# Performance work log

Hardware: AMD Instinct MI355X
Metric: run time of the kernel (lower is better)

## Reference

```python
import jax, jax.numpy as jnp
import numpy as np

MAX_THRESHOLD = 0.95


def leaky_clamp(x, lo, hi, slope):
    # identity inside [lo, hi], linear with `slope` outside
    return jnp.where(x < lo, lo + slope * (x - lo),
                     jnp.where(x > hi, hi + slope * (x - hi), x))


def or_gate_layer(x, W, tau_adder):
    # x: (B, in), W: (out, in)
    in_f = W.shape[1]
    tau_floor = float(np.log(in_f - 1) + np.log(MAX_THRESHOLD) - np.log(1.0 - MAX_THRESHOLD))
    tau = tau_floor + jax.nn.leaky_relu(tau_adder, negative_slope=0.05)
    aw = leaky_clamp(W, 0.0, 1.0, 0.1)           # (out, in)
    z = x[:, None, :] * aw[None, :, :]           # (B, out, in) broadcast
    p = jax.nn.softmax(tau * z, axis=-1)         # tau-scaled softmax over in
    return jnp.sum(p * z, axis=-1)               # (B, out)


def setup_inputs() -> dict:
    key = jax.random.key(0)
    ks = jax.random.split(key, 9)
    input_dim = 512
    layer_dims = [1024, 512, 256, 128]
    x = jax.random.uniform(ks[0], (128, input_dim), dtype=jnp.float32)
    in_dim = input_dim * 2
    out = {"x": x}
    for i, out_dim in enumerate(layer_dims):
        out[f"W{i}"] = jax.random.normal(ks[1 + i], (out_dim, in_dim), dtype=jnp.float32)
        out[f"tau{i}"] = jnp.zeros((), dtype=jnp.float32)
        in_dim = out_dim  # only_inverter=True
    return out


def reference(x, W0, W1, W2, W3, tau0, tau1, tau2, tau3):
    h = jnp.concatenate([x, 1.0 - x], axis=-1)   # pass_invert
    for W, t in ((W0, tau0), (W1, tau1), (W2, tau2), (W3, tau3)):
        h = 1.0 - or_gate_layer(h, W, t)         # only_inverter: invert after every layer
    return h
```

## Files before the change

### kernel.cpp

```cpp
#include <hip/hip_runtime.h>
#include <math.h>

#if defined(__has_builtin)
#  if __has_builtin(__builtin_amdgcn_exp2f)
#    define EXP2F(x) __builtin_amdgcn_exp2f(x)
#  endif
#endif
#ifndef EXP2F
#  define EXP2F(x) __expf(0.69314718055994530942f * (x))
#endif

template <int IN, int OUT, int BB, bool FIRST>
__launch_bounds__(256)
__global__ void or_layer(const float* __restrict__ hin,
                         const float* __restrict__ W,
                         const float* __restrict__ tau_ptr,
                         float* __restrict__ hout,
                         float tau_floor) {
  constexpr int OBB = 2;
  constexpr int NIT = IN / 64;
  constexpr int nOT = OUT / 32;

  const int lane = threadIdx.x & 63;
  const int wid  = threadIdx.x >> 6;
  const int il   = lane & 15;
  const int og   = lane >> 4;

  const int ot = blockIdx.x % nOT;
  const int bt = blockIdx.x / nOT;
  const int b0 = bt * BB;
  const int o0 = ot * 32 + wid * 8 + og * OBB;

  const float ta  = tau_ptr[0];
  const float tau = tau_floor + (ta >= 0.0f ? ta : 0.05f * ta);
  const float c2  = tau * 1.44269504088896340736f;

  const float4* __restrict__ Wv = (const float4*)W;
  const float4* __restrict__ Hv = (const float4*)hin;

  float s[BB][OBB], t[BB][OBB];
#pragma unroll
  for (int r = 0; r < BB; ++r)
#pragma unroll
    for (int c = 0; c < OBB; ++c) { s[r][c] = 0.0f; t[r][c] = 0.0f; }

#pragma unroll 2
  for (int ic = 0; ic < NIT; ++ic) {
    const int i4 = ic * 16 + il;

    float hc[BB][4];
    if (FIRST) {
      constexpr int HALF4 = IN / 8;
      if (i4 < HALF4) {
#pragma unroll
        for (int r = 0; r < BB; ++r) {
          float4 v = Hv[(b0 + r) * HALF4 + i4];
          hc[r][0] = v.x; hc[r][1] = v.y; hc[r][2] = v.z; hc[r][3] = v.w;
        }
      } else {
#pragma unroll
        for (int r = 0; r < BB; ++r) {
          float4 v = Hv[(b0 + r) * HALF4 + (i4 - HALF4)];
          hc[r][0] = 1.0f - v.x; hc[r][1] = 1.0f - v.y;
          hc[r][2] = 1.0f - v.z; hc[r][3] = 1.0f - v.w;
        }
      }
    } else {
#pragma unroll
      for (int r = 0; r < BB; ++r) {
        float4 v = Hv[(b0 + r) * (IN / 4) + i4];
        hc[r][0] = v.x; hc[r][1] = v.y; hc[r][2] = v.z; hc[r][3] = v.w;
      }
    }

    float cw[OBB][4];
#pragma unroll
    for (int c = 0; c < OBB; ++c) {
      float4 v = Wv[(o0 + c) * (IN / 4) + i4];
      float wj[4] = {v.x, v.y, v.z, v.w};
#pragma unroll
      for (int j = 0; j < 4; ++j) {
        const float m  = fminf(fmaxf(wj[j], 0.0f), 1.0f);
        const float aw = fmaf(0.1f, wj[j] - m, m);
        cw[c][j] = c2 * aw;
      }
    }

#pragma unroll
    for (int r = 0; r < BB; ++r)
#pragma unroll
      for (int c = 0; c < OBB; ++c)
#pragma unroll
        for (int j = 0; j < 4; ++j) {
          const float arg = cw[c][j] * hc[r][j];
          const float e   = EXP2F(arg);
          s[r][c] += e;
          t[r][c]  = fmaf(arg, e, t[r][c]);
        }
  }

#pragma unroll
  for (int m = 1; m < 16; m <<= 1) {
#pragma unroll
    for (int r = 0; r < BB; ++r)
#pragma unroll
      for (int c = 0; c < OBB; ++c) {
        s[r][c] += __shfl_xor(s[r][c], m, 64);
        t[r][c] += __shfl_xor(t[r][c], m, 64);
      }
  }

  if (il == 0) {
    const float inv_c2 = 1.0f / c2;
#pragma unroll
    for (int r = 0; r < BB; ++r)
#pragma unroll
      for (int c = 0; c < OBB; ++c) {
        const float out = t[r][c] / s[r][c] * inv_c2;
        hout[(b0 + r) * OUT + (o0 + c)] = 1.0f - out;
      }
  }
}

extern "C" void kernel_launch(void* const* d_in, const int* in_sizes, int n_in,
                              void* d_out, int out_size, void* d_ws, size_t ws_size,
                              hipStream_t stream) {
  const float* x    = (const float*)d_in[0];
  const float* W0   = (const float*)d_in[1];
  const float* tau0 = (const float*)d_in[2];
  const float* W1   = (const float*)d_in[3];
  const float* tau1 = (const float*)d_in[4];
  const float* W2   = (const float*)d_in[5];
  const float* tau2 = (const float*)d_in[6];
  const float* W3   = (const float*)d_in[7];
  const float* tau3 = (const float*)d_in[8];

  float* h1  = (float*)d_ws;
  float* h2  = h1 + 128 * 1024;
  float* h3  = h2 + 128 * 512;
  float* out = (float*)d_out;

  const double LOGR = 2.9444389791664403;
  const float tf1024 = (float)(log(1023.0) + LOGR);
  const float tf512  = (float)(log(511.0)  + LOGR);
  const float tf256  = (float)(log(255.0)  + LOGR);

  or_layer<1024, 1024, 8, true ><<<32 * 16, 256, 0, stream>>>(x,  W0, tau0, h1,  tf1024);
  or_layer<1024,  512, 8, false><<<16 * 16, 256, 0, stream>>>(h1, W1, tau1, h2,  tf1024);
  or_layer< 512,  256, 4, false><<< 8 * 32, 256, 0, stream>>>(h2, W2, tau2, h3,  tf512);
  or_layer< 256,  128, 2, false><<< 4 * 64, 256, 0, stream>>>(h3, W3, tau3, out, tf256);
}
```

Measured before the change: 124.7 us.

## Split exp2 between hardware transcendental unit and packed-FP32 polynomial emulation

Rewrites the inner loop on float2 vectors so the weight clamp, the multiplies and the accumulations can map to packed FP32 instructions. Half of the exponentials still use the hardware exp2 instruction. The other half use a degree-3 polynomial with exponent bit manipulation built from packed FMAs, which balances work between the transcendental unit and the vector ALU. It also drops the loop unroll to 1, and the launch grid sizes are only written as literals. The polynomial exp2 is less accurate than the hardware one and has no overflow or underflow guard.

```diff
diff --git a/kernel.cpp b/kernel.cpp
--- a/kernel.cpp
+++ b/kernel.cpp
@@ -9,6 +9,49 @@
 #ifndef EXP2F
 #  define EXP2F(x) __expf(0.69314718055994530942f * (x))
 #endif
+
+typedef float v2f __attribute__((ext_vector_type(2)));
+typedef int   v2i __attribute__((ext_vector_type(2)));
+
+__device__ __forceinline__ v2f v2fma(v2f a, v2f b, v2f c) {
+#if defined(__has_builtin) && __has_builtin(__builtin_elementwise_fma)
+  return __builtin_elementwise_fma(a, b, c);
+#else
+  v2f r; r.x = fmaf(a.x, b.x, c.x); r.y = fmaf(a.y, b.y, c.y); return r;
+#endif
+}
+__device__ __forceinline__ v2f v2max(v2f a, v2f b) {
+#if defined(__has_builtin) && __has_builtin(__builtin_elementwise_max)
+  return __builtin_elementwise_max(a, b);
+#else
+  v2f r; r.x = fmaxf(a.x, b.x); r.y = fmaxf(a.y, b.y); return r;
+#endif
+}
+__device__ __forceinline__ v2f v2min(v2f a, v2f b) {
+#if defined(__has_builtin) && __has_builtin(__builtin_elementwise_min)
+  return __builtin_elementwise_min(a, b);
+#else
+  v2f r; r.x = fminf(a.x, b.x); r.y = fminf(a.y, b.y); return r;
+#endif
+}
+
+__device__ __forceinline__ v2f fast_exp2_v2(v2f x) {
+  const v2f M  = {12582912.0f, 12582912.0f};
+  const v2f C2 = {0.055504109f, 0.055504109f};
+  const v2f C1 = {0.24022651f, 0.24022651f};
+  const v2f C0 = {0.69314718f, 0.69314718f};
+  const v2f ONE = {1.0f, 1.0f};
+  v2f y = x + M;
+  v2f n = y - M;
+  v2f f = x - n;
+  v2f p = v2fma(f, C2, C1);
+  p = v2fma(f, p, C0);
+  p = v2fma(f, p, ONE);
+  v2i yi = __builtin_bit_cast(v2i, y);
+  v2i pi = __builtin_bit_cast(v2i, p);
+  v2i r  = (yi << 23) + pi;
+  return __builtin_bit_cast(v2f, r);
+}
 
 template <int IN, int OUT, int BB, bool FIRST>
 __launch_bounds__(256)
@@ -34,79 +77,109 @@
   const float ta  = tau_ptr[0];
   const float tau = tau_floor + (ta >= 0.0f ? ta : 0.05f * ta);
   const float c2  = tau * 1.44269504088896340736f;
+  const v2f   c2v = {c2, c2};
+  const v2f   ZERO = {0.0f, 0.0f};
+  const v2f   ONE  = {1.0f, 1.0f};
+  const v2f   SLOPE = {0.1f, 0.1f};
 
   const float4* __restrict__ Wv = (const float4*)W;
   const float4* __restrict__ Hv = (const float4*)hin;
 
-  float s[BB][OBB], t[BB][OBB];
+  v2f s[BB][OBB], t[BB][OBB];
 #pragma unroll
   for (int r = 0; r < BB; ++r)
 #pragma unroll
-    for (int c = 0; c < OBB; ++c) { s[r][c] = 0.0f; t[r][c] = 0.0f; }
-
-#pragma unroll 2
+    for (int c = 0; c < OBB; ++c) {
+      s[r][c] = ZERO;
+      t[r][c] = ZERO;
+    }
+
+#pragma unroll 1
   for (int ic = 0; ic < NIT; ++ic) {
     const int i4 = ic * 16 + il;
 
-    float hc[BB][4];
+    v2f hp[BB][2];
     if (FIRST) {
       constexpr int HALF4 = IN / 8;
       if (i4 < HALF4) {
 #pragma unroll
         for (int r = 0; r < BB; ++r) {
           float4 v = Hv[(b0 + r) * HALF4 + i4];
-          hc[r][0] = v.x; hc[r][1] = v.y; hc[r][2] = v.z; hc[r][3] = v.w;
+          v2f a; a.x = v.x; a.y = v.y;
+          v2f b; b.x = v.z; b.y = v.w;
+          hp[r][0] = a; hp[r][1] = b;
         }
       } else {
 #pragma unroll
         for (int r = 0; r < BB; ++r) {
           float4 v = Hv[(b0 + r) * HALF4 + (i4 - HALF4)];
-          hc[r][0] = 1.0f - v.x; hc[r][1] = 1.0f - v.y;
-          hc[r][2] = 1.0f - v.z; hc[r][3] = 1.0f - v.w;
+          v2f a; a.x = v.x; a.y = v.y;
+          v2f b; b.x = v.z; b.y = v.w;
+          hp[r][0] = ONE - a; hp[r][1] = ONE - b;
         }
       }
     } else {
 #pragma unroll
       for (int r = 0; r < BB; ++r) {
         float4 v = Hv[(b0 + r) * (IN / 4) + i4];
-        hc[r][0] = v.x; hc[r][1] = v.y; hc[r][2] = v.z; hc[r][3] = v.w;
-      }
-    }
-
-    float cw[OBB][4];
+        v2f a; a.x = v.x; a.y = v.y;
+        v2f b; b.x = v.z; b.y = v.w;
+        hp[r][0] = a; hp[r][1] = b;
+      }
+    }
+
+    v2f cw[OBB][2];
 #pragma unroll
     for (int c = 0; c < OBB; ++c) {
       float4 v = Wv[(o0 + c) * (IN / 4) + i4];
-      float wj[4] = {v.x, v.y, v.z, v.w};
-#pragma unroll
-      for (int j = 0; j < 4; ++j) {
-        const float m  = fminf(fmaxf(wj[j], 0.0f), 1.0f);
-        const float aw = fmaf(0.1f, wj[j] - m, m);
-        cw[c][j] = c2 * aw;
+      v2f wp0; wp0.x = v.x; wp0.y = v.y;
+      v2f wp1; wp1.x = v.z; wp1.y = v.w;
+      v2f wp[2] = {wp0, wp1};
+#pragma unroll
+      for (int q = 0; q < 2; ++q) {
+        v2f m  = v2min(v2max(wp[q], ZERO), ONE);
+        v2f aw = v2fma(wp[q] - m, SLOPE, m);
+        cw[c][q] = aw * c2v;
       }
     }
 
 #pragma unroll
     for (int r = 0; r < BB; ++r)
 #pragma unroll
-      for (int c = 0; c < OBB; ++c)
-#pragma unroll
-        for (int j = 0; j < 4; ++j) {
-          const float arg = cw[c][j] * hc[r][j];
-          const float e   = EXP2F(arg);
+      for (int c = 0; c < OBB; ++c) {
+        {
+          v2f arg = cw[c][0] * hp[r][0];
+          v2f e;
+          e.x = EXP2F(arg.x);
+          e.y = EXP2F(arg.y);
           s[r][c] += e;
-          t[r][c]  = fmaf(arg, e, t[r][c]);
-        }
+          t[r][c]  = v2fma(arg, e, t[r][c]);
+        }
+        {
+          v2f arg = cw[c][1] * hp[r][1];
+          v2f e   = fast_exp2_v2(arg);
+          s[r][c] += e;
+          t[r][c]  = v2fma(arg, e, t[r][c]);
+        }
+      }
   }
 
+  float ss[BB][OBB], tt[BB][OBB];
+#pragma unroll
+  for (int r = 0; r < BB; ++r)
+#pragma unroll
+    for (int c = 0; c < OBB; ++c) {
+      ss[r][c] = s[r][c].x + s[r][c].y;
+      tt[r][c] = t[r][c].x + t[r][c].y;
+    }
 #pragma unroll
   for (int m = 1; m < 16; m <<= 1) {
 #pragma unroll
     for (int r = 0; r < BB; ++r)
 #pragma unroll
       for (int c = 0; c < OBB; ++c) {
-        s[r][c] += __shfl_xor(s[r][c], m, 64);
-        t[r][c] += __shfl_xor(t[r][c], m, 64);
+        ss[r][c] += __shfl_xor(ss[r][c], m, 64);
+        tt[r][c] += __shfl_xor(tt[r][c], m, 64);
       }
   }
 
@@ -116,7 +189,7 @@
     for (int r = 0; r < BB; ++r)
 #pragma unroll
       for (int c = 0; c < OBB; ++c) {
-        const float out = t[r][c] / s[r][c] * inv_c2;
+        const float out = tt[r][c] / ss[r][c] * inv_c2;
         hout[(b0 + r) * OUT + (o0 + c)] = 1.0f - out;
       }
   }
@@ -145,8 +218,8 @@
   const float tf512  = (float)(log(511.0)  + LOGR);
   const float tf256  = (float)(log(255.0)  + LOGR);
 
-  or_layer<1024, 1024, 8, true ><<<32 * 16, 256, 0, stream>>>(x,  W0, tau0, h1,  tf1024);
-  or_layer<1024,  512, 8, false><<<16 * 16, 256, 0, stream>>>(h1, W1, tau1, h2,  tf1024);
-  or_layer< 512,  256, 4, false><<< 8 * 32, 256, 0, stream>>>(h2, W2, tau2, h3,  tf512);
-  or_layer< 256,  128, 2, false><<< 4 * 64, 256, 0, stream>>>(h3, W3, tau3, out, tf256);
-}
+  or_layer<1024, 1024, 8, true ><<<512, 256, 0, stream>>>(x,  W0, tau0, h1,  tf1024);
+  or_layer<1024,  512, 8, false><<<256, 256, 0, stream>>>(h1, W1, tau1, h2,  tf1024);
+  or_layer< 512,  256, 4, false><<<256, 256, 0, stream>>>(h2, W2, tau2, h3,  tf512);
+  or_layer< 256,  128, 2, false><<<256, 256, 0, stream>>>(h3, W3, tau3, out, tf256);
+}
```

Result: slower. 137.8 us (+10.6%).

## Fuse all layers into one cooperative kernel with precomputed scaled weights

Applied to the files above, without the earlier changes.

Replaces the four per-layer launches with a single cooperative kernel that uses grid-wide syncs between layers. A prologue pass writes the clamped, tau-scaled weights to a workspace buffer, so the inner loops no longer redo the leaky clamp per batch tile. The cost is an extra full read and write of all weights, plus four grid barriers. If the cooperative launch fails, it falls back to a prep kernel followed by separate layer kernels.

```diff
diff --git a/kernel.cpp b/kernel.cpp
--- a/kernel.cpp
+++ b/kernel.cpp
@@ -1,5 +1,8 @@
 #include <hip/hip_runtime.h>
+#include <hip/hip_cooperative_groups.h>
 #include <math.h>
+
+namespace cg = cooperative_groups;
 
 #if defined(__has_builtin)
 #  if __has_builtin(__builtin_amdgcn_exp2f)
@@ -10,32 +13,53 @@
 #  define EXP2F(x) __expf(0.69314718055994530942f * (x))
 #endif
 
+
+__device__ __forceinline__ float calc_c2(const float* tau_ptr, float tf) {
+  const float ta  = tau_ptr[0];
+  const float tau = tf + (ta >= 0.0f ? ta : 0.05f * ta);
+  return tau * 1.44269504088896340736f;
+}
+
+__device__ __forceinline__ void prep_cw(const float* __restrict__ W,
+                                        float* __restrict__ cw,
+                                        int n4, float c2, int gtid, int gsz) {
+  const float4* __restrict__ Wv = (const float4*)W;
+  float4* __restrict__ Cv = (float4*)cw;
+  for (int k = gtid; k < n4; k += gsz) {
+    float4 v = Wv[k];
+    float w[4] = {v.x, v.y, v.z, v.w};
+    float o[4];
+#pragma unroll
+    for (int j = 0; j < 4; ++j) {
+      const float m  = fminf(fmaxf(w[j], 0.0f), 1.0f);
+      const float aw = fmaf(0.1f, w[j] - m, m);
+      o[j] = c2 * aw;
+    }
+    float4 r; r.x = o[0]; r.y = o[1]; r.z = o[2]; r.w = o[3];
+    Cv[k] = r;
+  }
+}
+
 template <int IN, int OUT, int BB, bool FIRST>
-__launch_bounds__(256)
-__global__ void or_layer(const float* __restrict__ hin,
-                         const float* __restrict__ W,
-                         const float* __restrict__ tau_ptr,
-                         float* __restrict__ hout,
-                         float tau_floor) {
+__device__ __forceinline__ void layer_body(const float* __restrict__ hin,
+                                           const float* __restrict__ cw,
+                                           float* __restrict__ hout,
+                                           float c2, int bid, int tid) {
   constexpr int OBB = 2;
   constexpr int NIT = IN / 64;
   constexpr int nOT = OUT / 32;
 
-  const int lane = threadIdx.x & 63;
-  const int wid  = threadIdx.x >> 6;
+  const int lane = tid & 63;
+  const int wid  = tid >> 6;
   const int il   = lane & 15;
   const int og   = lane >> 4;
 
-  const int ot = blockIdx.x % nOT;
-  const int bt = blockIdx.x / nOT;
+  const int ot = bid % nOT;
+  const int bt = bid / nOT;
   const int b0 = bt * BB;
   const int o0 = ot * 32 + wid * 8 + og * OBB;
 
-  const float ta  = tau_ptr[0];
-  const float tau = tau_floor + (ta >= 0.0f ? ta : 0.05f * ta);
-  const float c2  = tau * 1.44269504088896340736f;
-
-  const float4* __restrict__ Wv = (const float4*)W;
+  const float4* __restrict__ Cv = (const float4*)cw;
   const float4* __restrict__ Hv = (const float4*)hin;
 
   float s[BB][OBB], t[BB][OBB];
@@ -73,17 +97,11 @@
       }
     }
 
-    float cw[OBB][4];
+    float a[OBB][4];
 #pragma unroll
     for (int c = 0; c < OBB; ++c) {
-      float4 v = Wv[(o0 + c) * (IN / 4) + i4];
-      float wj[4] = {v.x, v.y, v.z, v.w};
-#pragma unroll
-      for (int j = 0; j < 4; ++j) {
-        const float m  = fminf(fmaxf(wj[j], 0.0f), 1.0f);
-        const float aw = fmaf(0.1f, wj[j] - m, m);
-        cw[c][j] = c2 * aw;
-      }
+      float4 v = Cv[(o0 + c) * (IN / 4) + i4];
+      a[c][0] = v.x; a[c][1] = v.y; a[c][2] = v.z; a[c][3] = v.w;
     }
 
 #pragma unroll
@@ -92,7 +110,7 @@
       for (int c = 0; c < OBB; ++c)
 #pragma unroll
         for (int j = 0; j < 4; ++j) {
-          const float arg = cw[c][j] * hc[r][j];
+          const float arg = a[c][j] * hc[r][j];
           const float e   = EXP2F(arg);
           s[r][c] += e;
           t[r][c]  = fmaf(arg, e, t[r][c]);
@@ -120,6 +138,69 @@
         hout[(b0 + r) * OUT + (o0 + c)] = 1.0f - out;
       }
   }
+}
+
+__launch_bounds__(256, 2)
+__global__ void or_fused(const float* __restrict__ x,
+                         const float* __restrict__ W0, const float* __restrict__ W1,
+                         const float* __restrict__ W2, const float* __restrict__ W3,
+                         const float* __restrict__ tau0, const float* __restrict__ tau1,
+                         const float* __restrict__ tau2, const float* __restrict__ tau3,
+                         float* __restrict__ h1, float* __restrict__ h2,
+                         float* __restrict__ h3, float* __restrict__ out,
+                         float* __restrict__ cw0, float* __restrict__ cw1,
+                         float* __restrict__ cw2, float* __restrict__ cw3,
+                         float tf0, float tf1, float tf2, float tf3) {
+  cg::grid_group grid = cg::this_grid();
+  const int tid  = threadIdx.x;
+  const int bid  = blockIdx.x;
+  const int gtid = bid * 256 + tid;
+  const int gsz  = gridDim.x * 256;
+
+  const float c2_0 = calc_c2(tau0, tf0);
+  const float c2_1 = calc_c2(tau1, tf1);
+  const float c2_2 = calc_c2(tau2, tf2);
+  const float c2_3 = calc_c2(tau3, tf3);
+
+  prep_cw(W0, cw0, 1024 * 1024 / 4, c2_0, gtid, gsz);
+  prep_cw(W1, cw1,  512 * 1024 / 4, c2_1, gtid, gsz);
+  prep_cw(W2, cw2,  256 *  512 / 4, c2_2, gtid, gsz);
+  prep_cw(W3, cw3,  128 *  256 / 4, c2_3, gtid, gsz);
+  grid.sync();
+
+  layer_body<1024, 1024, 8, true >(x, cw0, h1, c2_0, bid, tid);
+  grid.sync();
+  if (bid < 256) layer_body<1024, 512, 8, false>(h1, cw1, h2, c2_1, bid, tid);
+  grid.sync();
+  if (bid < 256) layer_body<512, 256, 4, false>(h2, cw2, h3, c2_2, bid, tid);
+  grid.sync();
+  if (bid < 256) layer_body<256, 128, 2, false>(h3, cw3, out, c2_3, bid, tid);
+}
+
+__launch_bounds__(256)
+__global__ void prep_all(const float* __restrict__ W0, const float* __restrict__ W1,
+                         const float* __restrict__ W2, const float* __restrict__ W3,
+                         const float* __restrict__ tau0, const float* __restrict__ tau1,
+                         const float* __restrict__ tau2, const float* __restrict__ tau3,
+                         float* __restrict__ cw0, float* __restrict__ cw1,
+                         float* __restrict__ cw2, float* __restrict__ cw3,
+                         float tf0, float tf1, float tf2, float tf3) {
+  const int gtid = blockIdx.x * 256 + threadIdx.x;
+  const int gsz  = gridDim.x * 256;
+  prep_cw(W0, cw0, 1024 * 1024 / 4, calc_c2(tau0, tf0), gtid, gsz);
+  prep_cw(W1, cw1,  512 * 1024 / 4, calc_c2(tau1, tf1), gtid, gsz);
+  prep_cw(W2, cw2,  256 *  512 / 4, calc_c2(tau2, tf2), gtid, gsz);
+  prep_cw(W3, cw3,  128 *  256 / 4, calc_c2(tau3, tf3), gtid, gsz);
+}
+
+template <int IN, int OUT, int BB, bool FIRST>
+__launch_bounds__(256)
+__global__ void or_layer_k(const float* __restrict__ hin,
+                           const float* __restrict__ cw,
+                           const float* __restrict__ tau_ptr,
+                           float* __restrict__ hout, float tf) {
+  layer_body<IN, OUT, BB, FIRST>(hin, cw, hout, calc_c2(tau_ptr, tf),
+                                 blockIdx.x, threadIdx.x);
 }
 
 extern "C" void kernel_launch(void* const* d_in, const int* in_sizes, int n_in,
@@ -138,15 +219,34 @@
   float* h1  = (float*)d_ws;
   float* h2  = h1 + 128 * 1024;
   float* h3  = h2 + 128 * 512;
+  float* cw0 = h3 + 128 * 256;
+  float* cw1 = cw0 + 1024 * 1024;
+  float* cw2 = cw1 + 512 * 1024;
+  float* cw3 = cw2 + 256 * 512;
   float* out = (float*)d_out;
 
   const double LOGR = 2.9444389791664403;
-  const float tf1024 = (float)(log(1023.0) + LOGR);
-  const float tf512  = (float)(log(511.0)  + LOGR);
-  const float tf256  = (float)(log(255.0)  + LOGR);
-
-  or_layer<1024, 1024, 8, true ><<<32 * 16, 256, 0, stream>>>(x,  W0, tau0, h1,  tf1024);
-  or_layer<1024,  512, 8, false><<<16 * 16, 256, 0, stream>>>(h1, W1, tau1, h2,  tf1024);
-  or_layer< 512,  256, 4, false><<< 8 * 32, 256, 0, stream>>>(h2, W2, tau2, h3,  tf512);
-  or_layer< 256,  128, 2, false><<< 4 * 64, 256, 0, stream>>>(h3, W3, tau3, out, tf256);
-}
+  float tf0 = (float)(log(1023.0) + LOGR);
+  float tf1 = (float)(log(1023.0) + LOGR);
+  float tf2 = (float)(log(511.0)  + LOGR);
+  float tf3 = (float)(log(255.0)  + LOGR);
+
+  void* args[] = {
+    (void*)&x,
+    (void*)&W0, (void*)&W1, (void*)&W2, (void*)&W3,
+    (void*)&tau0, (void*)&tau1, (void*)&tau2, (void*)&tau3,
+    (void*)&h1, (void*)&h2, (void*)&h3, (void*)&out,
+    (void*)&cw0, (void*)&cw1, (void*)&cw2, (void*)&cw3,
+    (void*)&tf0, (void*)&tf1, (void*)&tf2, (void*)&tf3,
+  };
+  hipError_t err = hipLaunchCooperativeKernel((void*)or_fused, dim3(512),
+                                              dim3(256), args, 0, stream);
+  if (err != hipSuccess) {
+    prep_all<<<256, 256, 0, stream>>>(W0, W1, W2, W3, tau0, tau1, tau2, tau3,
+                                      cw0, cw1, cw2, cw3, tf0, tf1, tf2, tf3);
+    or_layer_k<1024, 1024, 8, true ><<<512, 256, 0, stream>>>(x,  cw0, tau0, h1,  tf0);
+    or_layer_k<1024,  512, 8, false><<<256, 256, 0, stream>>>(h1, cw1, tau1, h2,  tf1);
+    or_layer_k< 512,  256, 4, false><<<256, 256, 0, stream>>>(h2, cw2, tau2, h3,  tf2);
+    or_layer_k< 256,  128, 2, false><<<256, 256, 0, stream>>>(h3, cw3, tau3, out, tf3);
+  }
+}
```

After: 331.8 us. 2.66x slower.
